# Kernel optimization log

Measured on AMD Instinct MI355X. Metric: run time of the kernel, lower is better.

Reference implementation:

```python
import jax, jax.numpy as jnp
import numpy as np

VOCAB = 50000
D_EMB = 300
N_BINS = 11
B, LQ, LD = 64, 32, 1024
MU = np.array([1.0, 0.9, 0.7, 0.5, 0.3, 0.1, -0.1, -0.3, -0.5, -0.7, -0.9], dtype=np.float32)
SIGMA = np.array([1e-3] + [0.1] * 10, dtype=np.float32)


def setup_inputs() -> dict:
    key = jax.random.key(0)
    ks = jax.random.split(key, 8)
    inputs_q = jax.random.randint(ks[0], (B, LQ), 0, VOCAB, dtype=jnp.int64 if jax.config.jax_enable_x64 else jnp.int32)
    inputs_d = jax.random.randint(ks[1], (B, LD), 0, VOCAB, dtype=jnp.int64 if jax.config.jax_enable_x64 else jnp.int32)
    mask_q = jnp.ones((B, LQ), dtype=jnp.float32)
    mask_d = jnp.ones((B, LD), dtype=jnp.float32)
    word_emb = jax.random.normal(ks[2], (VOCAB, D_EMB), dtype=jnp.float32) * 0.1
    attn_table = jax.random.uniform(ks[3], (VOCAB, 1), dtype=jnp.float32)  # frozen IDF embedding
    idf_w = jax.random.normal(ks[4], (1, 1), dtype=jnp.float32)
    idf_b = jnp.zeros((1,), dtype=jnp.float32)
    dense_w = jax.random.normal(ks[5], (1, N_BINS), dtype=jnp.float32) * 0.1
    dense_b = jnp.zeros((1,), dtype=jnp.float32)
    return {
        'inputs_q': inputs_q, 'inputs_d': inputs_d,
        'mask_q': mask_q, 'mask_d': mask_d,
        'word_emb': word_emb, 'attn_table': attn_table,
        'idf_w': idf_w, 'idf_b': idf_b,
        'dense_w': dense_w, 'dense_b': dense_b,
    }


def _l2_normalize(x, eps=1e-12):
    # matches F.normalize(x, 2, dim=-1): x / max(||x||, eps)
    n = jnp.sqrt(jnp.sum(x * x, axis=-1, keepdims=True))
    return x / jnp.maximum(n, eps)


def reference(inputs_q, inputs_d, mask_q, mask_d, word_emb, attn_table,
              idf_w, idf_b, dense_w, dense_b):
    mu = jnp.asarray(MU)        # [K]
    sigma = jnp.asarray(SIGMA)  # [K]
    # idf attention on query tokens: Linear(1,1) on frozen embedding lookup
    attn_q = attn_table[inputs_q] * idf_w[0, 0] + idf_b[0]          # [B,Lq,1]
    q_embed = _l2_normalize(word_emb[inputs_q])                      # [B,Lq,E]
    d_embed = _l2_normalize(word_emb[inputs_d])                      # [B,Ld,E]
    sim = jnp.einsum('bqe,bde->bqd', q_embed, d_embed)               # [B,Lq,Ld]
    # RBF soft-histogram over n_bins kernels, doc tokens masked
    rbf = jnp.exp(-((sim[..., None] - mu) ** 2) / (sigma ** 2) / 2)  # [B,Lq,Ld,K]
    pooling_sum = jnp.einsum('bqdk,bd->bqk', rbf, mask_d)            # [B,Lq,K]
    wq = mask_q[..., None] * attn_q                                   # [B,Lq,1]
    log_pool = jnp.log(jnp.clip(pooling_sum, 1e-10)) * wq * 0.01     # [B,Lq,K]
    log_pooling_sum = jnp.sum(log_pool, axis=1)                      # [B,K]
    out = jnp.tanh(log_pooling_sum @ dense_w.T + dense_b)            # [B,1]
    return out[:, 0]                                                 # [B]
```

## Files before the change

kernel.cpp:

```cpp
#include <hip/hip_runtime.h>
#include <math.h>

#define VOCAB  50000
#define D_EMB  300
#define NBINS  11
#define BATCH  64
#define LQ     32
#define LD     1024
#define DTILE  64
#define NDT    (LD / DTILE)
#define NSTEP  10
#define KPAD   320

typedef __attribute__((ext_vector_type(8))) short short8;
typedef __attribute__((ext_vector_type(4))) float floatx4;

__constant__ float c_mu[NBINS]  = {1.0f, 0.9f, 0.7f, 0.5f, 0.3f, 0.1f,
                                   -0.1f, -0.3f, -0.5f, -0.7f, -0.9f};
__constant__ float c_is2[NBINS] = {500000.0f, 50.f, 50.f, 50.f, 50.f, 50.f,
                                   50.f, 50.f, 50.f, 50.f, 50.f};

static __device__ __forceinline__ unsigned short f32_bf16(float f) {
  unsigned u = __float_as_uint(f);
  u += 0x7FFFu + ((u >> 16) & 1u);
  return (unsigned short)(u >> 16);
}
static __device__ __forceinline__ float bf16_f32(unsigned short h) {
  return __uint_as_float(((unsigned)h) << 16);
}

__global__ __launch_bounds__(256) void knrm_vocab(
    const float* __restrict__ word_emb, short* __restrict__ emb_bf16,
    float* __restrict__ invnorm)
{
  const int row = blockIdx.x * 16 + (threadIdx.x >> 4);
  const int j   = threadIdx.x & 15;
  const float4* src = (const float4*)(word_emb + (size_t)row * D_EMB);
  short* dst = emb_bf16 + (size_t)row * KPAD;
  float p = 0.f;
#pragma unroll
  for (int cc = 0; cc < 3; ++cc) {
    const int c = j + 16 * cc;
    if (c < 40) {
      float4 fa = make_float4(0.f, 0.f, 0.f, 0.f);
      float4 fb = make_float4(0.f, 0.f, 0.f, 0.f);
      if (8 * c < D_EMB)     fa = src[2 * c];
      if (8 * c + 4 < D_EMB) fb = src[2 * c + 1];
      unsigned short h[8];
      h[0] = f32_bf16(fa.x); h[1] = f32_bf16(fa.y);
      h[2] = f32_bf16(fa.z); h[3] = f32_bf16(fa.w);
      h[4] = f32_bf16(fb.x); h[5] = f32_bf16(fb.y);
      h[6] = f32_bf16(fb.z); h[7] = f32_bf16(fb.w);
      short8 v;
#pragma unroll
      for (int t = 0; t < 8; ++t) {
        const float x = bf16_f32(h[t]);
        p += x * x;
        v[t] = (short)h[t];
      }
      *(short8*)(dst + 8 * c) = v;
    }
  }
  p += __shfl_xor(p, 1); p += __shfl_xor(p, 2);
  p += __shfl_xor(p, 4); p += __shfl_xor(p, 8);
  if (j == 0) invnorm[row] = 1.f / fmaxf(sqrtf(p), 1e-12f);
}

__global__ __launch_bounds__(256) void knrm_main(
    const int* __restrict__ inputs_q, const int* __restrict__ inputs_d,
    const float* __restrict__ mask_d, const short* __restrict__ emb_bf16,
    const float* __restrict__ invnorm, float* __restrict__ partial)
{
  const int b    = blockIdx.y;
  const int dt   = blockIdx.x;
  const int tid  = threadIdx.x;
  const int wid  = tid >> 6;
  const int lane = tid & 63;
  const int khi  = lane >> 4;
  const int rl   = lane & 15;
  const int qt   = wid >> 1;
  const int dp   = wid & 1;

  __shared__ float red[4][16][NBINS];

  const int dbase = b * LD + dt * DTILE;
  const int tq  = inputs_q[b * LQ + 16 * qt + rl];
  const int td0 = inputs_d[dbase + 32 * dp + rl];
  const int td1 = inputs_d[dbase + 32 * dp + 16 + rl];
  const short8* arow = (const short8*)(emb_bf16 + (size_t)tq  * KPAD);
  const short8* b0r  = (const short8*)(emb_bf16 + (size_t)td0 * KPAD);
  const short8* b1r  = (const short8*)(emb_bf16 + (size_t)td1 * KPAD);

  floatx4 acc0 = {0.f, 0.f, 0.f, 0.f};
  floatx4 acc1 = {0.f, 0.f, 0.f, 0.f};
#pragma unroll
  for (int s = 0; s < NSTEP; ++s) {
    const short8 a  = arow[4 * s + khi];
    const short8 b0 = b0r [4 * s + khi];
    const short8 b1 = b1r [4 * s + khi];
    acc0 = __builtin_amdgcn_mfma_f32_16x16x32_bf16(a, b0, acc0, 0, 0, 0);
    acc1 = __builtin_amdgcn_mfma_f32_16x16x32_bf16(a, b1, acc1, 0, 0, 0);
  }

  const float iq_own = invnorm[tq];
  float iq[4];
#pragma unroll
  for (int r = 0; r < 4; ++r) iq[r] = __shfl(iq_own, 4 * khi + r);
  const float id0 = invnorm[td0], id1 = invnorm[td1];
  const float md0 = mask_d[dbase + 32 * dp + rl];
  const float md1 = mask_d[dbase + 32 * dp + 16 + rl];

  float ps[4][NBINS];
#pragma unroll
  for (int r = 0; r < 4; ++r) {
    const float s0 = acc0[r] * iq[r] * id0;
    const float s1 = acc1[r] * iq[r] * id1;
#pragma unroll
    for (int k = 0; k < NBINS; ++k) {
      const float d0 = s0 - c_mu[k];
      const float d1 = s1 - c_mu[k];
      ps[r][k] = md0 * __expf(-d0 * d0 * c_is2[k])
               + md1 * __expf(-d1 * d1 * c_is2[k]);
    }
  }

#pragma unroll
  for (int off = 1; off < 16; off <<= 1)
#pragma unroll
    for (int r = 0; r < 4; ++r)
#pragma unroll
      for (int k = 0; k < NBINS; ++k)
        ps[r][k] += __shfl_xor(ps[r][k], off);

  if (rl == 0)
#pragma unroll
    for (int r = 0; r < 4; ++r)
#pragma unroll
      for (int k = 0; k < NBINS; ++k)
        red[wid][4 * khi + r][k] = ps[r][k];
  __syncthreads();

  for (int v = tid; v < LQ * NBINS; v += 256) {
    const int q = v / NBINS, k = v % NBINS;
    const float sv = (q < 16) ? (red[0][q][k] + red[1][q][k])
                              : (red[2][q - 16][k] + red[3][q - 16][k]);
    partial[((size_t)(b * LQ + q) * NBINS + k) * NDT + dt] = sv;
  }
}

__global__ __launch_bounds__(128) void knrm_finalize(
    const float* __restrict__ partial, const int* __restrict__ inputs_q,
    const float* __restrict__ mask_q, const float* __restrict__ attn_table,
    const float* __restrict__ idf_w, const float* __restrict__ idf_b,
    const float* __restrict__ dense_w, const float* __restrict__ dense_b,
    float* __restrict__ out)
{
  const int b   = blockIdx.x;
  const int tid = threadIdx.x;
  __shared__ float pool[LQ][NBINS];
  __shared__ float wq_s[LQ];
  __shared__ float lps[NBINS];

  for (int v = tid; v < LQ * NBINS; v += 128) {
    const int q = v / NBINS, k = v % NBINS;
    const float* p = partial + ((size_t)(b * LQ + q) * NBINS + k) * NDT;
    float s = 0.f;
#pragma unroll
    for (int t = 0; t < NDT; ++t) s += p[t];
    pool[q][k] = logf(fmaxf(s, 1e-10f));
  }
  if (tid < LQ) {
    const int tok = inputs_q[b * LQ + tid];
    wq_s[tid] = mask_q[b * LQ + tid] * (attn_table[tok] * idf_w[0] + idf_b[0]);
  }
  __syncthreads();
  if (tid < NBINS) {
    float s = 0.f;
    for (int q = 0; q < LQ; ++q) s += pool[q][tid] * wq_s[q];
    lps[tid] = 0.01f * s;
  }
  __syncthreads();
  if (tid == 0) {
    float z = dense_b[0];
    for (int k = 0; k < NBINS; ++k) z += lps[k] * dense_w[k];
    out[b] = tanhf(z);
  }
}

extern "C" void kernel_launch(void* const* d_in, const int* in_sizes, int n_in,
                              void* d_out, int out_size, void* d_ws, size_t ws_size,
                              hipStream_t stream) {
  const int*   inputs_q  = (const int*)d_in[0];
  const int*   inputs_d  = (const int*)d_in[1];
  const float* mask_q    = (const float*)d_in[2];
  const float* mask_d    = (const float*)d_in[3];
  const float* word_emb  = (const float*)d_in[4];
  const float* attn_tab  = (const float*)d_in[5];
  const float* idf_w     = (const float*)d_in[6];
  const float* idf_b     = (const float*)d_in[7];
  const float* dense_w   = (const float*)d_in[8];
  const float* dense_b   = (const float*)d_in[9];
  float* out = (float*)d_out;

  char*  ws       = (char*)d_ws;
  float* partial  = (float*)ws;
  short* emb_bf16 = (short*)(ws + (2u  << 20));
  float* invnorm  = (float*)(ws + (36u << 20));

  knrm_vocab<<<VOCAB / 16, 256, 0, stream>>>(word_emb, emb_bf16, invnorm);
  dim3 grid(NDT, BATCH);
  knrm_main<<<grid, 256, 0, stream>>>(inputs_q, inputs_d, mask_d,
                                      emb_bf16, invnorm, partial);
  knrm_finalize<<<BATCH, 128, 0, stream>>>(partial, inputs_q, mask_q, attn_tab,
                                           idf_w, idf_b, dense_w, dense_b, out);
}
```

Measured before the change: 138.0 us.

## Gather token embeddings into MFMA fragment layout instead of converting whole vocab

Replaces the whole-vocabulary bf16 conversion kernel with a per-batch expand kernel. It gathers only the query and document tokens' embeddings, converts them to bf16, and writes them pre-swizzled in MFMA fragment order along with per-token inverse norms. The main kernel then reads contiguous, lane-coalesced fragments instead of indirect row gathers. The cost is that repeated tokens are converted multiple times, and the gathered count (~67k rows) exceeds the vocabulary size, so total traffic may not shrink.

```diff
diff --git a/kernel.cpp b/kernel.cpp
--- a/kernel.cpp
+++ b/kernel.cpp
@@ -10,7 +10,7 @@
 #define DTILE  64
 #define NDT    (LD / DTILE)
 #define NSTEP  10
-#define KPAD   320
+#define FRAG_SHORTS (NSTEP * 512)
 
 typedef __attribute__((ext_vector_type(8))) short short8;
 typedef __attribute__((ext_vector_type(4))) float floatx4;
@@ -29,47 +29,70 @@
   return __uint_as_float(((unsigned)h) << 16);
 }
 
-__global__ __launch_bounds__(256) void knrm_vocab(
-    const float* __restrict__ word_emb, short* __restrict__ emb_bf16,
-    float* __restrict__ invnorm)
-{
-  const int row = blockIdx.x * 16 + (threadIdx.x >> 4);
-  const int j   = threadIdx.x & 15;
-  const float4* src = (const float4*)(word_emb + (size_t)row * D_EMB);
-  short* dst = emb_bf16 + (size_t)row * KPAD;
+static __device__ __forceinline__ float stage_rows(
+    const float* __restrict__ emb_row,
+    short* __restrict__ region, int khi, int lane)
+{
+  const float4* emb4 = (const float4*)emb_row;
   float p = 0.f;
 #pragma unroll
-  for (int cc = 0; cc < 3; ++cc) {
-    const int c = j + 16 * cc;
-    if (c < 40) {
-      float4 fa = make_float4(0.f, 0.f, 0.f, 0.f);
-      float4 fb = make_float4(0.f, 0.f, 0.f, 0.f);
-      if (8 * c < D_EMB)     fa = src[2 * c];
-      if (8 * c + 4 < D_EMB) fb = src[2 * c + 1];
-      unsigned short h[8];
-      h[0] = f32_bf16(fa.x); h[1] = f32_bf16(fa.y);
-      h[2] = f32_bf16(fa.z); h[3] = f32_bf16(fa.w);
-      h[4] = f32_bf16(fb.x); h[5] = f32_bf16(fb.y);
-      h[6] = f32_bf16(fb.z); h[7] = f32_bf16(fb.w);
-      short8 v;
-#pragma unroll
-      for (int t = 0; t < 8; ++t) {
-        const float x = bf16_f32(h[t]);
-        p += x * x;
-        v[t] = (short)h[t];
-      }
-      *(short8*)(dst + 8 * c) = v;
+  for (int s = 0; s < NSTEP; ++s) {
+    const int k0 = 32 * s + 8 * khi;
+    float4 fa = make_float4(0.f, 0.f, 0.f, 0.f);
+    float4 fb = make_float4(0.f, 0.f, 0.f, 0.f);
+    if (k0 < D_EMB)     fa = emb4[k0 >> 2];
+    if (k0 + 4 < D_EMB) fb = emb4[(k0 >> 2) + 1];
+    unsigned short h[8];
+    h[0] = f32_bf16(fa.x); h[1] = f32_bf16(fa.y);
+    h[2] = f32_bf16(fa.z); h[3] = f32_bf16(fa.w);
+    h[4] = f32_bf16(fb.x); h[5] = f32_bf16(fb.y);
+    h[6] = f32_bf16(fb.z); h[7] = f32_bf16(fb.w);
+    short8 v;
+#pragma unroll
+    for (int j = 0; j < 8; ++j) {
+      const float x = bf16_f32(h[j]);
+      p += x * x;
+      v[j] = (short)h[j];
     }
-  }
-  p += __shfl_xor(p, 1); p += __shfl_xor(p, 2);
-  p += __shfl_xor(p, 4); p += __shfl_xor(p, 8);
-  if (j == 0) invnorm[row] = 1.f / fmaxf(sqrtf(p), 1e-12f);
+    *(short8*)(region + s * 512 + lane * 8) = v;
+  }
+  return p;
+}
+
+__global__ __launch_bounds__(256) void knrm_expand(
+    const int* __restrict__ inputs_q, const int* __restrict__ inputs_d,
+    const float* __restrict__ word_emb, short* __restrict__ afrag,
+    short* __restrict__ dfrag, float* __restrict__ invq,
+    float* __restrict__ invd)
+{
+  const int b    = blockIdx.y;
+  const int i    = blockIdx.x * 4 + (threadIdx.x >> 6);
+  const int lane = threadIdx.x & 63;
+  const int khi  = lane >> 4, rl = lane & 15;
+  if (i >= 66) return;
+
+  int tok; short* dst;
+  if (i < 2) {
+    tok = inputs_q[b * LQ + i * 16 + rl];
+    dst = afrag + (size_t)(b * 2 + i) * FRAG_SHORTS;
+  } else {
+    const int g = i - 2;
+    tok = inputs_d[b * LD + g * 16 + rl];
+    dst = dfrag + (size_t)(b * 64 + g) * FRAG_SHORTS;
+  }
+  float p = stage_rows(word_emb + (size_t)tok * D_EMB, dst, khi, lane);
+  p += __shfl_xor(p, 16); p += __shfl_xor(p, 32);
+  if (lane < 16) {
+    const float inv = 1.f / fmaxf(sqrtf(p), 1e-12f);
+    if (i < 2) invq[b * LQ + i * 16 + lane] = inv;
+    else       invd[b * LD + (i - 2) * 16 + lane] = inv;
+  }
 }
 
 __global__ __launch_bounds__(256) void knrm_main(
-    const int* __restrict__ inputs_q, const int* __restrict__ inputs_d,
-    const float* __restrict__ mask_d, const short* __restrict__ emb_bf16,
-    const float* __restrict__ invnorm, float* __restrict__ partial)
+    const float* __restrict__ mask_d, const short* __restrict__ afrag,
+    const short* __restrict__ dfrag, const float* __restrict__ invq,
+    const float* __restrict__ invd, float* __restrict__ partial)
 {
   const int b    = blockIdx.y;
   const int dt   = blockIdx.x;
@@ -83,30 +106,28 @@
 
   __shared__ float red[4][16][NBINS];
 
-  const int dbase = b * LD + dt * DTILE;
-  const int tq  = inputs_q[b * LQ + 16 * qt + rl];
-  const int td0 = inputs_d[dbase + 32 * dp + rl];
-  const int td1 = inputs_d[dbase + 32 * dp + 16 + rl];
-  const short8* arow = (const short8*)(emb_bf16 + (size_t)tq  * KPAD);
-  const short8* b0r  = (const short8*)(emb_bf16 + (size_t)td0 * KPAD);
-  const short8* b1r  = (const short8*)(emb_bf16 + (size_t)td1 * KPAD);
+  const short8* arow = (const short8*)(afrag + (size_t)(b * 2 + qt) * FRAG_SHORTS);
+  const short8* b0r  = (const short8*)(dfrag + (size_t)(b * 64 + dt * 4 + 2 * dp) * FRAG_SHORTS);
+  const short8* b1r  = b0r + FRAG_SHORTS / 8;
 
   floatx4 acc0 = {0.f, 0.f, 0.f, 0.f};
   floatx4 acc1 = {0.f, 0.f, 0.f, 0.f};
 #pragma unroll
   for (int s = 0; s < NSTEP; ++s) {
-    const short8 a  = arow[4 * s + khi];
-    const short8 b0 = b0r [4 * s + khi];
-    const short8 b1 = b1r [4 * s + khi];
+    const short8 a  = arow[s * 64 + lane];
+    const short8 b0 = b0r [s * 64 + lane];
+    const short8 b1 = b1r [s * 64 + lane];
     acc0 = __builtin_amdgcn_mfma_f32_16x16x32_bf16(a, b0, acc0, 0, 0, 0);
     acc1 = __builtin_amdgcn_mfma_f32_16x16x32_bf16(a, b1, acc1, 0, 0, 0);
   }
 
-  const float iq_own = invnorm[tq];
+  const int dbase = b * LD + dt * DTILE;
+  const float iq_own = invq[b * LQ + 16 * qt + rl];
   float iq[4];
 #pragma unroll
   for (int r = 0; r < 4; ++r) iq[r] = __shfl(iq_own, 4 * khi + r);
-  const float id0 = invnorm[td0], id1 = invnorm[td1];
+  const float id0 = invd[dbase + 32 * dp + rl];
+  const float id1 = invd[dbase + 32 * dp + 16 + rl];
   const float md0 = mask_d[dbase + 32 * dp + rl];
   const float md1 = mask_d[dbase + 32 * dp + 16 + rl];
 
@@ -202,15 +223,18 @@
   const float* dense_b   = (const float*)d_in[9];
   float* out = (float*)d_out;
 
-  char*  ws       = (char*)d_ws;
-  float* partial  = (float*)ws;
-  short* emb_bf16 = (short*)(ws + (2u  << 20));
-  float* invnorm  = (float*)(ws + (36u << 20));
-
-  knrm_vocab<<<VOCAB / 16, 256, 0, stream>>>(word_emb, emb_bf16, invnorm);
+  char*  ws      = (char*)d_ws;
+  float* partial = (float*)ws;
+  short* afrag   = (short*)(ws + (2u  << 20));
+  short* dfrag   = (short*)(ws + (4u  << 20));
+  float* invq    = (float*)(ws + (48u << 20));
+  float* invd    = (float*)(ws + (49u << 20));
+
+  dim3 egrid(17, BATCH);
+  knrm_expand<<<egrid, 256, 0, stream>>>(inputs_q, inputs_d, word_emb,
+                                         afrag, dfrag, invq, invd);
   dim3 grid(NDT, BATCH);
-  knrm_main<<<grid, 256, 0, stream>>>(inputs_q, inputs_d, mask_d,
-                                      emb_bf16, invnorm, partial);
+  knrm_main<<<grid, 256, 0, stream>>>(mask_d, afrag, dfrag, invq, invd, partial);
   knrm_finalize<<<BATCH, 128, 0, stream>>>(partial, inputs_q, mask_q, attn_tab,
                                            idf_w, idf_b, dense_w, dense_b, out);
 }
```

Measured after the change: 146.5 us. 6.2% more time.
